# Kernel tuning notes

Measured on AMD Instinct MI355X. Metric: run time of the kernel, lower is better.

## Reference

```python
import jax, jax.numpy as jnp
import numpy as np

DIM = 768
HEADS = 12
E = 8
TOPK = 2
EPS = 1e-5


def layer_norm(x, g, b):
    m = jnp.mean(x, axis=-1, keepdims=True)
    v = jnp.mean((x - m) ** 2, axis=-1, keepdims=True)
    return (x - m) * jax.lax.rsqrt(v + EPS) * g + b


def setup_inputs() -> dict:
    key = jax.random.key(0)
    ks = jax.random.split(key, 12)
    B, N, C = 16, 1024, DIM
    s = 0.02
    return {
        "x": jax.random.normal(ks[0], (B, N, C), jnp.float32),
        "noise": jax.random.normal(ks[1], (B, N, E), jnp.float32),
        "ln1_g": jnp.ones((C,), jnp.float32),
        "ln1_b": jnp.zeros((C,), jnp.float32),
        "qkv_w": jax.random.normal(ks[2], (C, 3 * C), jnp.float32) * s,  # pre-transposed
        "proj_w": jax.random.normal(ks[3], (C, C), jnp.float32) * s,
        "proj_b": jnp.zeros((C,), jnp.float32),
        "ln2_g": jnp.ones((C,), jnp.float32),
        "ln2_b": jnp.zeros((C,), jnp.float32),
        "route_w": jax.random.normal(ks[4], (C, E), jnp.float32) * s,
        "route_b": jnp.zeros((E,), jnp.float32),
        "rln_g": jnp.ones((E,), jnp.float32),
        "rln_b": jnp.zeros((E,), jnp.float32),
        "expert_w": jax.random.normal(ks[5], (E, C, C), jnp.float32) * s,  # [E, in, out]
        "expert_b": jnp.zeros((E, C), jnp.float32),
    }


def reference(x, noise, ln1_g, ln1_b, qkv_w, proj_w, proj_b, ln2_g, ln2_b,
              route_w, route_b, rln_g, rln_b, expert_w, expert_b):
    B, N, C = x.shape
    H = HEADS
    Dh = C // H
    scale = Dh ** -0.5

    # --- Attention branch ---
    h = layer_norm(x, ln1_g, ln1_b)
    qkv = (h @ qkv_w).reshape(B, N, 3, H, Dh)
    q, k, v = qkv[:, :, 0], qkv[:, :, 1], qkv[:, :, 2]  # [B,N,H,Dh]
    attn = jnp.einsum('bnhd,bmhd->bhnm', q, k) * scale
    attn = jax.nn.softmax(attn, axis=-1)
    o = jnp.einsum('bhnm,bmhd->bnhd', attn, v).reshape(B, N, C)
    x = x + o @ proj_w + proj_b

    # --- MoE branch ---
    h = layer_norm(x, ln2_g, ln2_b)
    logits = layer_norm(h @ route_w + route_b, rln_g, rln_b)  # [B,N,E]
    rw = jax.nn.softmax(logits, axis=-1) + noise * (1.0 / E)
    topk_w, topk_idx = jax.lax.top_k(rw, TOPK)               # [B,N,K]
    topk_w = jax.nn.softmax(topk_w, axis=-1)

    # dense all-expert compute (faithful to source): [B,N,E,C]
    expert_out = jnp.einsum('bnc,ecd->bned', h, expert_w) + expert_b
    selected = jnp.take_along_axis(expert_out, topk_idx[..., None], axis=2)  # [B,N,K,C]
    moe = jnp.sum(selected * topk_w[..., None], axis=2)
    return x + moe
```

## Files before the change

### kernel.cpp

```cpp
#include <hip/hip_runtime.h>
#include <hip/hip_fp16.h>

typedef unsigned short u16;
typedef unsigned int u32;
typedef _Float16 f16;
typedef short bf16x8 __attribute__((ext_vector_type(8)));
typedef f16 f16x8 __attribute__((ext_vector_type(8)));
typedef float f32x4 __attribute__((ext_vector_type(4)));
typedef u32 u32x4 __attribute__((ext_vector_type(4)));

#define TOKENS 16384
#define CDIM 768
#define NEXP 8

__device__ __forceinline__ float b2f(u16 u) {
  return __uint_as_float(((u32)u) << 16);
}
__device__ __forceinline__ u16 f2b(float f) {
  u32 u = __float_as_uint(f);
  return (u16)((u + 0x7fffu + ((u >> 16) & 1u)) >> 16);
}
__device__ __forceinline__ f32x4 mfma_bf(bf16x8 a, bf16x8 b, f32x4 c) {
  return __builtin_amdgcn_mfma_f32_16x16x32_bf16(a, b, c, 0, 0, 0);
}
__device__ __forceinline__ f32x4 mfma_h(f16x8 a, f16x8 b, f32x4 c) {
  return __builtin_amdgcn_mfma_f32_16x16x32_f16(a, b, c, 0, 0, 0);
}
__device__ __forceinline__ void split8(const float* v, f16x8& h, f16x8& l) {
#pragma unroll
  for (int i = 0; i < 8; i++) {
    const f16 hh = (f16)v[i];
    h[i] = hh;
    l[i] = (f16)(v[i] - (float)hh);
  }
}

__global__ __launch_bounds__(256) void transpose_split_f16(
    const float* __restrict__ in, f16* __restrict__ oh, f16* __restrict__ ol,
    int K, int N) {
  __shared__ float tile[64][65];
  const int n0 = blockIdx.x * 64, k0 = blockIdx.y * 64;
#pragma unroll
  for (int i = 0; i < 16; i++) {
    const int s = threadIdx.x + i * 256;
    const int r = s >> 6, c = s & 63;
    tile[r][c] = in[(size_t)(k0 + r) * N + n0 + c];
  }
  __syncthreads();
#pragma unroll
  for (int i = 0; i < 16; i++) {
    const int s = threadIdx.x + i * 256;
    const int r = s >> 6, c = s & 63;
    const float v = tile[c][r];
    const f16 h = (f16)v;
    oh[(size_t)(n0 + r) * K + k0 + c] = h;
    ol[(size_t)(n0 + r) * K + k0 + c] = (f16)(v - (float)h);
  }
}

__global__ __launch_bounds__(256) void transpose_f32_bf16(
    const float* __restrict__ in, u16* __restrict__ out, int K, int N) {
  __shared__ u16 tile[64][65];
  const int z = blockIdx.z;
  in += (size_t)z * K * N;
  out += (size_t)z * K * N;
  const int n0 = blockIdx.x * 64, k0 = blockIdx.y * 64;
#pragma unroll
  for (int i = 0; i < 16; i++) {
    const int s = threadIdx.x + i * 256;
    const int r = s >> 6, c = s & 63;
    tile[r][c] = f2b(in[(size_t)(k0 + r) * N + n0 + c]);
  }
  __syncthreads();
#pragma unroll
  for (int i = 0; i < 16; i++) {
    const int s = threadIdx.x + i * 256;
    const int r = s >> 6, c = s & 63;
    out[(size_t)(n0 + r) * K + k0 + c] = tile[c][r];
  }
}

template <bool BF16OUT>
__global__ __launch_bounds__(256) void ln_rows(const float* __restrict__ in,
                                               const float* __restrict__ g,
                                               const float* __restrict__ bt,
                                               void* __restrict__ out) {
  const int row = blockIdx.x * 4 + (threadIdx.x >> 6);
  const int lane = threadIdx.x & 63;
  const size_t base = (size_t)row * CDIM;
  float v[12];
  float s = 0.f, ss = 0.f;
#pragma unroll
  for (int j = 0; j < 12; j++) {
    const int idx = lane + j * 64;
    v[j] = in[base + idx];
    s += v[j];
    ss += v[j] * v[j];
  }
#pragma unroll
  for (int m = 1; m < 64; m <<= 1) {
    s += __shfl_xor(s, m);
    ss += __shfl_xor(ss, m);
  }
  const float mean = s * (1.f / CDIM);
  const float var = ss * (1.f / CDIM) - mean * mean;
  const float rs = rsqrtf(var + 1e-5f);
#pragma unroll
  for (int j = 0; j < 12; j++) {
    const int idx = lane + j * 64;
    const float y = (v[j] - mean) * rs * g[idx] + bt[idx];
    if (BF16OUT)
      ((u16*)out)[base + idx] = f2b(y);
    else
      ((float*)out)[base + idx] = y;
  }
}

template <int EPI>
__global__ __launch_bounds__(256) void gemm_f16s(
    const float* __restrict__ A, const f16* __restrict__ Bth,
    const f16* __restrict__ Btl, float* __restrict__ C, int M, int N, int K,
    const float* __restrict__ bias, const float* __restrict__ xres) {
  __shared__ f16 Ah[128 * 64];
  __shared__ f16 Al[128 * 64];
  __shared__ f16 Bh[128 * 64];
  __shared__ f16 Bl[128 * 64];
  const int tid = threadIdx.x;
  const int lane = tid & 63, wv = tid >> 6;
  const int wr = wv >> 1, wc = wv & 1;
  const int lm = lane & 15, lq = lane >> 4;
  const int m0 = blockIdx.y * 128, n0 = blockIdx.x * 128;
  f32x4 acc[4][4];
  const f32x4 z4 = {0.f, 0.f, 0.f, 0.f};
#pragma unroll
  for (int i = 0; i < 4; i++)
#pragma unroll
    for (int j = 0; j < 4; j++) acc[i][j] = z4;

  for (int k0 = 0; k0 < K; k0 += 64) {
    __syncthreads();
#pragma unroll
    for (int i = 0; i < 4; i++) {
      const int s = tid + i * 256;
      const int r = s >> 3, g = s & 7;
      float av[8];
      *(float4*)&av[0] = *(const float4*)(A + (size_t)(m0 + r) * K + k0 + g * 8);
      *(float4*)&av[4] =
          *(const float4*)(A + (size_t)(m0 + r) * K + k0 + g * 8 + 4);
      f16x8 hh, ll;
      split8(av, hh, ll);
      const int sw = r * 64 + ((g ^ (r & 7)) << 3);
      *(f16x8*)(&Ah[sw]) = hh;
      *(f16x8*)(&Al[sw]) = ll;
      *(f16x8*)(&Bh[sw]) = *(const f16x8*)(Bth + (size_t)(n0 + r) * K + k0 + g * 8);
      *(f16x8*)(&Bl[sw]) = *(const f16x8*)(Btl + (size_t)(n0 + r) * K + k0 + g * 8);
    }
    __syncthreads();
#pragma unroll
    for (int kx = 0; kx < 8; kx += 4) {
      f16x8 afh[4], afl[4], bfh[4], bfl[4];
#pragma unroll
      for (int i = 0; i < 4; i++) {
        const int ra = wr * 64 + i * 16 + lm;
        const int aw = ra * 64 + (((ra & 7) ^ (kx + lq)) << 3);
        afh[i] = *(const f16x8*)(&Ah[aw]);
        afl[i] = *(const f16x8*)(&Al[aw]);
        const int rb = wc * 64 + i * 16 + lm;
        const int bw = rb * 64 + (((rb & 7) ^ (kx + lq)) << 3);
        bfh[i] = *(const f16x8*)(&Bh[bw]);
        bfl[i] = *(const f16x8*)(&Bl[bw]);
      }
#pragma unroll
      for (int i = 0; i < 4; i++)
#pragma unroll
        for (int j = 0; j < 4; j++) {
          acc[i][j] = mfma_h(afh[i], bfh[j], acc[i][j]);
          acc[i][j] = mfma_h(afh[i], bfl[j], acc[i][j]);
          acc[i][j] = mfma_h(afl[i], bfh[j], acc[i][j]);
        }
    }
  }
#pragma unroll
  for (int i = 0; i < 4; i++)
#pragma unroll
    for (int r = 0; r < 4; r++) {
      const size_t row = m0 + wr * 64 + i * 16 + lq * 4 + r;
#pragma unroll
      for (int j = 0; j < 4; j++) {
        const int col = n0 + wc * 64 + j * 16 + lm;
        float v = acc[i][j][r];
        if (EPI == 1) v += bias[col] + xres[row * N + col];
        C[row * N + col] = v;
      }
    }
}

__global__ __launch_bounds__(256) void attn_f16s(const float* __restrict__ qkvf,
                                                 float* __restrict__ o,
                                                 int qb) {
  __shared__ f16 Kh[64 * 64];
  __shared__ f16 Kl[64 * 64];
  __shared__ f16 Vh[64 * 64];
  __shared__ f16 Vl[64 * 64];
  __shared__ f16 Ph[4 * 16 * 64];
  __shared__ f16 Pl[4 * 16 * 64];
  const int bz = blockIdx.z, h = blockIdx.y, qt = blockIdx.x;
  const int tid = threadIdx.x, wv = tid >> 6, lane = tid & 63;
  const int lm = lane & 15, lq = lane >> 4;

  f16x8 qh[2], ql[2];
  {
    const size_t qbase =
        (size_t)(bz * 1024 + qt * 64 + wv * 16 + lm) * 2304 + h * 64;
#pragma unroll
    for (int f = 0; f < 2; f++) {
      float v[8];
      *(float4*)&v[0] = *(const float4*)(qkvf + qbase + f * 32 + lq * 8);
      *(float4*)&v[4] = *(const float4*)(qkvf + qbase + f * 32 + lq * 8 + 4);
      split8(v, qh[f], ql[f]);
    }
  }
  const f32x4 z4 = {0.f, 0.f, 0.f, 0.f};
  f32x4 oacc[4];
#pragma unroll
  for (int jb = 0; jb < 4; jb++) oacc[jb] = z4;
  float mrun[4], lrun[4];
#pragma unroll
  for (int r = 0; r < 4; r++) {
    mrun[r] = -1e30f;
    lrun[r] = 0.f;
  }
  const int vd = tid & 63;
  const int vkg = tid >> 6;
  f16* pwh = &Ph[wv * 16 * 64];
  f16* pwl = &Pl[wv * 16 * 64];

  for (int kt = 0; kt < 16; kt++) {
    __syncthreads();
#pragma unroll
    for (int i = 0; i < 2; i++) {
      const int s2 = tid + i * 256;
      const int r = s2 >> 3, g = s2 & 7;
      const size_t kb =
          (size_t)(bz * 1024 + kt * 64 + r) * 2304 + 768 + h * 64 + g * 8;
      float v[8];
      *(float4*)&v[0] = *(const float4*)(qkvf + kb);
      *(float4*)&v[4] = *(const float4*)(qkvf + kb + 4);
      f16x8 hh, ll;
      split8(v, hh, ll);
      const int sw = r * 64 + ((g ^ (r & 7)) << 3);
      *(f16x8*)(&Kh[sw]) = hh;
      *(f16x8*)(&Kl[sw]) = ll;
    }
#pragma unroll
    for (int sseg = 0; sseg < 2; sseg++) {
      const int k0v = vkg * 16 + sseg * 8;
      float v[8];
#pragma unroll
      for (int j = 0; j < 8; j++)
        v[j] = qkvf[(size_t)(bz * 1024 + kt * 64 + k0v + j) * 2304 + 1536 +
                    h * 64 + vd];
      f16x8 hh, ll;
      split8(v, hh, ll);
      const int g = k0v >> 3;
      const int sw = vd * 64 + ((g ^ (vd & 7)) << 3);
      *(f16x8*)(&Vh[sw]) = hh;
      *(f16x8*)(&Vl[sw]) = ll;
    }
    __syncthreads();

    f32x4 sa[4];
#pragma unroll
    for (int j = 0; j < 4; j++) sa[j] = z4;
#pragma unroll
    for (int kx = 0; kx < 8; kx += 4) {
      const f16x8 ah = qh[kx >> 2], al = ql[kx >> 2];
#pragma unroll
      for (int j = 0; j < 4; j++) {
        const int rb = j * 16 + lm;
        const int bw = rb * 64 + (((rb & 7) ^ (kx + lq)) << 3);
        const f16x8 bh = *(const f16x8*)(&Kh[bw]);
        const f16x8 bl = *(const f16x8*)(&Kl[bw]);
        sa[j] = mfma_h(ah, bh, sa[j]);
        sa[j] = mfma_h(ah, bl, sa[j]);
        sa[j] = mfma_h(al, bh, sa[j]);
      }
    }
#pragma unroll
    for (int j = 0; j < 4; j++)
#pragma unroll
      for (int r = 0; r < 4; r++) sa[j][r] *= 0.125f;

#pragma unroll
    for (int r = 0; r < 4; r++) {
      float mx = fmaxf(fmaxf(sa[0][r], sa[1][r]), fmaxf(sa[2][r], sa[3][r]));
      mx = fmaxf(mx, __shfl_xor(mx, 1));
      mx = fmaxf(mx, __shfl_xor(mx, 2));
      mx = fmaxf(mx, __shfl_xor(mx, 4));
      mx = fmaxf(mx, __shfl_xor(mx, 8));
      const float mnew = fmaxf(mrun[r], mx);
      const float alpha = expf(mrun[r] - mnew);
      float ps = 0.f;
#pragma unroll
      for (int j = 0; j < 4; j++) {
        const float p = expf(sa[j][r] - mnew);
        sa[j][r] = p;
        ps += p;
      }
      ps += __shfl_xor(ps, 1);
      ps += __shfl_xor(ps, 2);
      ps += __shfl_xor(ps, 4);
      ps += __shfl_xor(ps, 8);
      lrun[r] = lrun[r] * alpha + ps;
      mrun[r] = mnew;
#pragma unroll
      for (int jb = 0; jb < 4; jb++) oacc[jb][r] *= alpha;
    }

#pragma unroll
    for (int j = 0; j < 4; j++)
#pragma unroll
      for (int r = 0; r < 4; r++) {
        const int qr = lq * 4 + r;
        const int key = j * 16 + lm;
        const int ad = qr * 64 + (((qr & 7) ^ (key >> 3)) << 3) + (key & 7);
        const float p = sa[j][r];
        const f16 ph = (f16)p;
        pwh[ad] = ph;
        pwl[ad] = (f16)(p - (float)ph);
      }
#pragma unroll
    for (int kx2 = 0; kx2 < 8; kx2 += 4) {
      const int pw = lm * 64 + (((lm & 7) ^ (kx2 + lq)) << 3);
      const f16x8 pah = *(const f16x8*)(&pwh[pw]);
      const f16x8 pal = *(const f16x8*)(&pwl[pw]);
#pragma unroll
      for (int jb = 0; jb < 4; jb++) {
        const int rb = jb * 16 + lm;
        const int vw = rb * 64 + (((rb & 7) ^ (kx2 + lq)) << 3);
        const f16x8 vh = *(const f16x8*)(&Vh[vw]);
        const f16x8 vl = *(const f16x8*)(&Vl[vw]);
        oacc[jb] = mfma_h(pah, vh, oacc[jb]);
        oacc[jb] = mfma_h(pah, vl, oacc[jb]);
        oacc[jb] = mfma_h(pal, vh, oacc[jb]);
      }
    }
  }
  const int gtok = (qb * 4 + bz) * 1024 + qt * 64;
#pragma unroll
  for (int r = 0; r < 4; r++) {
    const float inv = 1.f / lrun[r];
    const size_t row = (size_t)gtok + wv * 16 + lq * 4 + r;
#pragma unroll
    for (int jb = 0; jb < 4; jb++) {
      const int col = h * 64 + jb * 16 + lm;
      o[row * CDIM + col] = oacc[jb][r] * inv;
    }
  }
}

__global__ __launch_bounds__(256) void gemm_expert(
    const u16* __restrict__ A, const u16* __restrict__ Bt,
    __half* __restrict__ Cp, int N, int K, const float* __restrict__ bias,
    const int* __restrict__ counts, const int* __restrict__ eBase,
    const int* __restrict__ tokList, const float* __restrict__ wgtList) {
  __shared__ u16 As[128 * 64];
  __shared__ u16 Bs[128 * 64];
  const int did = blockIdx.x;
  const int e = did & 7;
  const int s = did >> 3;
  const int bx = s % 6;
  const int by = s / 6;
  const int cnt = counts[e];
  const int m0 = by * 128, n0 = bx * 128;
  if (m0 >= cnt) return;
  const int tid = threadIdx.x;
  const int lane = tid & 63, wv = tid >> 6;
  const int wr = wv >> 1, wc = wv & 1;
  const int lm = lane & 15, lq = lane >> 4;
  const u16* Bte = Bt + (size_t)e * N * K;
  const int* tokl = tokList + e * TOKENS;
  const float* wl = wgtList + e * TOKENS;
  const float* biasE = bias + e * N;
  const int base0 = eBase[e];

  const int r0 = tid >> 3, g = tid & 7;
  const int swz = (g ^ (r0 & 7)) << 3;
  const u16* ap[4];
  const u16* bp[4];
#pragma unroll
  for (int i = 0; i < 4; i++) {
    const int row = m0 + r0 + i * 32;
    const int tok = (row < cnt) ? tokl[row] : 0;
    ap[i] = A + (size_t)tok * K + g * 8;
    bp[i] = Bte + (size_t)(n0 + r0 + i * 32) * K + g * 8;
  }

  f32x4 acc[4][4];
  const f32x4 z4 = {0.f, 0.f, 0.f, 0.f};
#pragma unroll
  for (int i = 0; i < 4; i++)
#pragma unroll
    for (int j = 0; j < 4; j++) acc[i][j] = z4;

  u32x4 pa[4], pb[4];
#pragma unroll
  for (int i = 0; i < 4; i++) {
    pa[i] = *(const u32x4*)(ap[i]);
    pb[i] = *(const u32x4*)(bp[i]);
  }
#pragma unroll
  for (int i = 0; i < 4; i++) {
    *(u32x4*)(&As[(r0 + i * 32) * 64 + swz]) = pa[i];
    *(u32x4*)(&Bs[(r0 + i * 32) * 64 + swz]) = pb[i];
  }

  for (int k0 = 0; k0 < K; k0 += 64) {
    __syncthreads();
    const bool more = (k0 + 64) < K;
    if (more) {
#pragma unroll
      for (int i = 0; i < 4; i++) {
        pa[i] = *(const u32x4*)(ap[i] + k0 + 64);
        pb[i] = *(const u32x4*)(bp[i] + k0 + 64);
      }
    }
#pragma unroll
    for (int kx = 0; kx < 8; kx += 4) {
      bf16x8 af[4], bfv[4];
#pragma unroll
      for (int i = 0; i < 4; i++) {
        const int ra = wr * 64 + i * 16 + lm;
        af[i] = *(const bf16x8*)(&As[ra * 64 + (((ra & 7) ^ (kx + lq)) << 3)]);
        const int rb = wc * 64 + i * 16 + lm;
        bfv[i] = *(const bf16x8*)(&Bs[rb * 64 + (((rb & 7) ^ (kx + lq)) << 3)]);
      }
#pragma unroll
      for (int i = 0; i < 4; i++)
#pragma unroll
        for (int j = 0; j < 4; j++)
          acc[i][j] = mfma_bf(af[i], bfv[j], acc[i][j]);
    }
    __syncthreads();
    if (more) {
#pragma unroll
      for (int i = 0; i < 4; i++) {
        *(u32x4*)(&As[(r0 + i * 32) * 64 + swz]) = pa[i];
        *(u32x4*)(&Bs[(r0 + i * 32) * 64 + swz]) = pb[i];
      }
    }
  }
#pragma unroll
  for (int i = 0; i < 4; i++)
#pragma unroll
    for (int r = 0; r < 4; r++) {
      const int rowi = m0 + wr * 64 + i * 16 + lq * 4 + r;
      const bool live = (rowi < cnt);
      const float w = live ? wl[rowi] : 0.f;
      const size_t prow = live ? (size_t)(base0 + rowi) * (size_t)N : 0;
#pragma unroll
      for (int j = 0; j < 4; j++) {
        const int col = n0 + wc * 64 + j * 16 + lm;
        const float v = (acc[i][j][r] + biasE[col]) * w;
        const float vn = __shfl_xor(v, 1);
        if (live && (lm & 1) == 0) {
          *(__half2*)(Cp + prow + col) =
              __halves2half2(__float2half(v), __float2half(vn));
        }
      }
    }
}

__global__ __launch_bounds__(256) void router_kernel(
    const float* __restrict__ x2, const float* __restrict__ g2,
    const float* __restrict__ b2, const float* __restrict__ rw,
    const float* __restrict__ rb, const float* __restrict__ rlng,
    const float* __restrict__ rlnb, const float* __restrict__ noise,
    int* __restrict__ eidx, float* __restrict__ ewgt) {
  const int token = blockIdx.x * 4 + (threadIdx.x >> 6);
  const int lane = threadIdx.x & 63;
  const size_t base = (size_t)token * CDIM;
  float v[12];
  float s = 0.f, ss = 0.f;
#pragma unroll
  for (int j = 0; j < 12; j++) {
    const int idx = lane + j * 64;
    v[j] = x2[base + idx];
    s += v[j];
    ss += v[j] * v[j];
  }
#pragma unroll
  for (int m = 1; m < 64; m <<= 1) {
    s += __shfl_xor(s, m);
    ss += __shfl_xor(ss, m);
  }
  const float mean = s * (1.f / CDIM);
  const float var = ss * (1.f / CDIM) - mean * mean;
  const float rs = rsqrtf(var + 1e-5f);

  float acc[8];
#pragma unroll
  for (int e = 0; e < 8; e++) acc[e] = 0.f;
#pragma unroll
  for (int j = 0; j < 12; j++) {
    const int d = lane + j * 64;
    const float hv = (v[j] - mean) * rs * g2[d] + b2[d];
    const f32x4 w0v = *(const f32x4*)(rw + (size_t)d * 8);
    const f32x4 w1v = *(const f32x4*)(rw + (size_t)d * 8 + 4);
#pragma unroll
    for (int e = 0; e < 4; e++) {
      acc[e] += hv * w0v[e];
      acc[e + 4] += hv * w1v[e];
    }
  }
#pragma unroll
  for (int m = 1; m < 64; m <<= 1)
#pragma unroll
    for (int e = 0; e < 8; e++) acc[e] += __shfl_xor(acc[e], m);

  float y[8];
  float emean = 0.f;
#pragma unroll
  for (int e = 0; e < 8; e++) {
    y[e] = acc[e] + rb[e];
    emean += y[e];
  }
  emean *= 0.125f;
  float evar = 0.f;
#pragma unroll
  for (int e = 0; e < 8; e++) {
    const float d = y[e] - emean;
    evar += d * d;
  }
  evar *= 0.125f;
  const float ers = rsqrtf(evar + 1e-5f);
  float lg[8];
  float mx = -1e30f;
#pragma unroll
  for (int e = 0; e < 8; e++) {
    lg[e] = (y[e] - emean) * ers * rlng[e] + rlnb[e];
    mx = fmaxf(mx, lg[e]);
  }
  float se = 0.f;
#pragma unroll
  for (int e = 0; e < 8; e++) {
    lg[e] = expf(lg[e] - mx);
    se += lg[e];
  }
  const float inv = 1.f / se;
  float r2[8];
#pragma unroll
  for (int e = 0; e < 8; e++)
    r2[e] = lg[e] * inv + noise[(size_t)token * 8 + e] * 0.125f;

  int e0 = 0;
  float v0 = r2[0];
#pragma unroll
  for (int e = 1; e < 8; e++)
    if (r2[e] > v0) {
      v0 = r2[e];
      e0 = e;
    }
  int e1 = -1;
  float v1 = -1e30f;
#pragma unroll
  for (int e = 0; e < 8; e++)
    if (e != e0 && r2[e] > v1) {
      v1 = r2[e];
      e1 = e;
    }
  const float w0 = 1.f / (1.f + expf(v1 - v0));
  if (lane == 0) {
    eidx[token * 2] = e0;
    eidx[token * 2 + 1] = e1;
    ewgt[token * 2] = w0;
    ewgt[token * 2 + 1] = 1.f - w0;
  }
}

__global__ __launch_bounds__(256) void build_lists(
    const int* __restrict__ eidx, const float* __restrict__ ewgt,
    int* __restrict__ counts, int* __restrict__ tokL, float* __restrict__ wgtL,
    int* __restrict__ posL) {
  const int e = blockIdx.x;
  __shared__ int cnt;
  if (threadIdx.x == 0) cnt = 0;
  __syncthreads();
  const int lane = threadIdx.x & 63;
  for (int t = threadIdx.x; t < TOKENS; t += 256) {
#pragma unroll
    for (int k = 0; k < 2; k++) {
      const bool match = (eidx[t * 2 + k] == e);
      const unsigned long long mb = __ballot(match);
      if (mb) {
        const int leader = __ffsll((unsigned long long)mb) - 1;
        int base = 0;
        if (lane == leader) base = atomicAdd(&cnt, __popcll(mb));
        base = __shfl(base, leader);
        if (match) {
          const int rank = __popcll(mb & ((1ull << lane) - 1ull));
          tokL[e * TOKENS + base + rank] = t;
          wgtL[e * TOKENS + base + rank] = ewgt[t * 2 + k];
          posL[t * 2 + k] = base + rank;
        }
      }
    }
  }
  __syncthreads();
  if (threadIdx.x == 0) counts[e] = cnt;
}

__global__ void prefix_counts(const int* __restrict__ counts,
                              int* __restrict__ eBase) {
  if (threadIdx.x == 0) {
    int s = 0;
#pragma unroll
    for (int e = 0; e < NEXP; e++) {
      eBase[e] = s;
      s += counts[e];
    }
    eBase[NEXP] = s;
  }
}

__global__ __launch_bounds__(256) void combine_moe(
    float* __restrict__ x2, const __half* __restrict__ Cp,
    const int* __restrict__ eidx, const int* __restrict__ posL,
    const int* __restrict__ eBase) {
  const int t = blockIdx.x * 4 + (threadIdx.x >> 6);
  const int lane = threadIdx.x & 63;
  const int e0 = eidx[t * 2], e1 = eidx[t * 2 + 1];
  const size_t q0 = (size_t)(eBase[e0] + posL[t * 2]) * CDIM;
  const size_t q1 = (size_t)(eBase[e1] + posL[t * 2 + 1]) * CDIM;
  const size_t base = (size_t)t * CDIM;
#pragma unroll
  for (int j = 0; j < 12; j++) {
    const int d = lane + j * 64;
    const float m =
        __half2float(Cp[q0 + d]) + __half2float(Cp[q1 + d]);
    x2[base + d] += m;
  }
}

__global__ __launch_bounds__(256) void copy_f32(const float* __restrict__ in,
                                                float* __restrict__ out) {
  const int i = (blockIdx.x * 256 + threadIdx.x) * 4;
  *(float4*)(out + i) = *(const float4*)(in + i);
}

extern "C" void kernel_launch(void* const* d_in, const int* in_sizes, int n_in,
                              void* d_out, int out_size, void* d_ws,
                              size_t ws_size, hipStream_t stream) {
  const float* x = (const float*)d_in[0];
  const float* noise = (const float*)d_in[1];
  const float* ln1_g = (const float*)d_in[2];
  const float* ln1_b = (const float*)d_in[3];
  const float* qkv_w = (const float*)d_in[4];
  const float* proj_w = (const float*)d_in[5];
  const float* proj_b = (const float*)d_in[6];
  const float* ln2_g = (const float*)d_in[7];
  const float* ln2_b = (const float*)d_in[8];
  const float* route_w = (const float*)d_in[9];
  const float* route_b = (const float*)d_in[10];
  const float* rln_g = (const float*)d_in[11];
  const float* rln_b = (const float*)d_in[12];
  const float* expert_w = (const float*)d_in[13];
  const float* expert_b = (const float*)d_in[14];

  char* ws = (char*)d_ws;
  float* x2f = (float*)(ws);
  float* qkvf = (float*)(ws + 50331648);
  u16* exp_wt = (u16*)(ws + 50331648);
  u16* h2 = (u16*)(ws + 59768832);
  int* counts = (int*)(ws + 84934656);
  int* eBase = (int*)(ws + 84934784);
  int* eidx = (int*)(ws + 84934912);
  float* ewgt = (float*)(ws + 85065984);
  int* tokL = (int*)(ws + 85197056);
  float* wgtL = (float*)(ws + 85721344);
  int* posL = (int*)(ws + 86245632);
  f16* qkvw_h = (f16*)(ws + 88080384);
  f16* qkvw_l = (f16*)(ws + 91619328);
  f16* projw_h = (f16*)(ws + 95158272);
  f16* projw_l = (f16*)(ws + 96337920);
  float* h1f = (float*)d_out;
  __half* cperm = (__half*)d_out;

  const dim3 blk(256);
  transpose_split_f16<<<dim3(36, 12), blk, 0, stream>>>(qkv_w, qkvw_h, qkvw_l,
                                                        768, 2304);
  transpose_split_f16<<<dim3(12, 12), blk, 0, stream>>>(proj_w, projw_h,
                                                        projw_l, 768, 768);
  ln_rows<false><<<dim3(4096), blk, 0, stream>>>(x, ln1_g, ln1_b, h1f);
  for (int q = 0; q < 4; q++) {
    gemm_f16s<0><<<dim3(18, 32), blk, 0, stream>>>(
        h1f + (size_t)q * 4096 * 768, qkvw_h, qkvw_l, qkvf, 4096, 2304, 768,
        nullptr, nullptr);
    attn_f16s<<<dim3(16, 12, 4), blk, 0, stream>>>(qkvf, h1f, q);
  }
  gemm_f16s<1><<<dim3(6, 128), blk, 0, stream>>>(h1f, projw_h, projw_l, x2f,
                                                 16384, 768, 768, proj_b, x);
  ln_rows<true><<<dim3(4096), blk, 0, stream>>>(x2f, ln2_g, ln2_b, h2);
  transpose_f32_bf16<<<dim3(12, 12, 8), blk, 0, stream>>>(expert_w, exp_wt,
                                                          768, 768);
  router_kernel<<<dim3(4096), blk, 0, stream>>>(x2f, ln2_g, ln2_b, route_w,
                                                route_b, rln_g, rln_b, noise,
                                                eidx, ewgt);
  build_lists<<<dim3(8), blk, 0, stream>>>(eidx, ewgt, counts, tokL, wgtL,
                                           posL);
  prefix_counts<<<dim3(1), dim3(64), 0, stream>>>(counts, eBase);
  gemm_expert<<<dim3(6144), blk, 0, stream>>>(h2, exp_wt, cperm, 768, 768,
                                              expert_b, counts, eBase, tokL,
                                              wgtL);
  combine_moe<<<dim3(4096), blk, 0, stream>>>(x2f, cperm, eidx, posL, eBase);
  copy_f32<<<dim3(12288), blk, 0, stream>>>(x2f, (float*)d_out);
}
```

Baseline: 1.140 ms.

## Fuse f16 hi/lo split and softmax scale into QKV GEMM epilogue

The QKV GEMM now writes Q and K directly as split f16 high/low halves, with Q pre-multiplied by scale*log2(e), and writes V as packed hi/lo u32 pairs. Previously it wrote fp32 that the attention kernel split on every tile load. The attention kernel loads the pre-split halves, drops its per-score scaling, and uses exp2f. This removes repeated conversion work and shrinks intermediate traffic, because each key/value tile is reloaded by many query blocks. The cost is scattered 2-byte stores in the GEMM epilogue and a slightly different rounding order, since Q is scaled before the split.

```diff
diff --git a/kernel.cpp b/kernel.cpp
--- a/kernel.cpp
+++ b/kernel.cpp
@@ -13,12 +13,16 @@
 #define CDIM 768
 #define NEXP 8
 
-__device__ __forceinline__ float b2f(u16 u) {
-  return __uint_as_float(((u32)u) << 16);
-}
+#define QSCALE 0.18033688011112043f
+
 __device__ __forceinline__ u16 f2b(float f) {
   u32 u = __float_as_uint(f);
   return (u16)((u + 0x7fffu + ((u >> 16) & 1u)) >> 16);
+}
+__device__ __forceinline__ u16 f16bits(f16 x) {
+  union { f16 f; u16 u; } c;
+  c.f = x;
+  return c.u;
 }
 __device__ __forceinline__ f32x4 mfma_bf(bf16x8 a, bf16x8 b, f32x4 c) {
   return __builtin_amdgcn_mfma_f32_16x16x32_bf16(a, b, c, 0, 0, 0);
@@ -120,7 +124,8 @@
 __global__ __launch_bounds__(256) void gemm_f16s(
     const float* __restrict__ A, const f16* __restrict__ Bth,
     const f16* __restrict__ Btl, float* __restrict__ C, int M, int N, int K,
-    const float* __restrict__ bias, const float* __restrict__ xres) {
+    const float* __restrict__ bias, const float* __restrict__ xres,
+    f16* __restrict__ Oh, f16* __restrict__ Ol, u32* __restrict__ Ov) {
   __shared__ f16 Ah[128 * 64];
   __shared__ f16 Al[128 * 64];
   __shared__ f16 Bh[128 * 64];
@@ -189,15 +194,30 @@
       for (int j = 0; j < 4; j++) {
         const int col = n0 + wc * 64 + j * 16 + lm;
         float v = acc[i][j][r];
-        if (EPI == 1) v += bias[col] + xres[row * N + col];
-        C[row * N + col] = v;
-      }
-    }
-}
-
-__global__ __launch_bounds__(256) void attn_f16s(const float* __restrict__ qkvf,
-                                                 float* __restrict__ o,
-                                                 int qb) {
+        if constexpr (EPI == 0) {
+          C[row * N + col] = v;
+        } else if constexpr (EPI == 1) {
+          v += bias[col] + xres[row * N + col];
+          C[row * N + col] = v;
+        } else {
+          if (n0 < 768) v *= QSCALE;
+          const f16 hh = (f16)v;
+          const f16 ll = (f16)(v - (float)hh);
+          if (n0 < 1536) {
+            Oh[row * 1536 + col] = hh;
+            Ol[row * 1536 + col] = ll;
+          } else {
+            Ov[row * 768 + (col - 1536)] =
+                (u32)f16bits(hh) | ((u32)f16bits(ll) << 16);
+          }
+        }
+      }
+    }
+}
+
+__global__ __launch_bounds__(256) void attn_f16s(
+    const f16* __restrict__ qkh, const f16* __restrict__ qkl,
+    const u32* __restrict__ vI, float* __restrict__ o, int qb) {
   __shared__ f16 Kh[64 * 64];
   __shared__ f16 Kl[64 * 64];
   __shared__ f16 Vh[64 * 64];
@@ -210,14 +230,12 @@
 
   f16x8 qh[2], ql[2];
   {
-    const size_t qbase =
-        (size_t)(bz * 1024 + qt * 64 + wv * 16 + lm) * 2304 + h * 64;
+    const size_t qrow =
+        (size_t)(bz * 1024 + qt * 64 + wv * 16 + lm) * 1536 + h * 64;
 #pragma unroll
     for (int f = 0; f < 2; f++) {
-      float v[8];
-      *(float4*)&v[0] = *(const float4*)(qkvf + qbase + f * 32 + lq * 8);
-      *(float4*)&v[4] = *(const float4*)(qkvf + qbase + f * 32 + lq * 8 + 4);
-      split8(v, qh[f], ql[f]);
+      qh[f] = *(const f16x8*)(qkh + qrow + f * 32 + lq * 8);
+      ql[f] = *(const f16x8*)(qkl + qrow + f * 32 + lq * 8);
     }
   }
   const f32x4 z4 = {0.f, 0.f, 0.f, 0.f};
@@ -242,26 +260,22 @@
       const int s2 = tid + i * 256;
       const int r = s2 >> 3, g = s2 & 7;
       const size_t kb =
-          (size_t)(bz * 1024 + kt * 64 + r) * 2304 + 768 + h * 64 + g * 8;
-      float v[8];
-      *(float4*)&v[0] = *(const float4*)(qkvf + kb);
-      *(float4*)&v[4] = *(const float4*)(qkvf + kb + 4);
-      f16x8 hh, ll;
-      split8(v, hh, ll);
+          (size_t)(bz * 1024 + kt * 64 + r) * 1536 + 768 + h * 64 + g * 8;
       const int sw = r * 64 + ((g ^ (r & 7)) << 3);
-      *(f16x8*)(&Kh[sw]) = hh;
-      *(f16x8*)(&Kl[sw]) = ll;
+      *(f16x8*)(&Kh[sw]) = *(const f16x8*)(qkh + kb);
+      *(f16x8*)(&Kl[sw]) = *(const f16x8*)(qkl + kb);
     }
 #pragma unroll
     for (int sseg = 0; sseg < 2; sseg++) {
       const int k0v = vkg * 16 + sseg * 8;
-      float v[8];
-#pragma unroll
-      for (int j = 0; j < 8; j++)
-        v[j] = qkvf[(size_t)(bz * 1024 + kt * 64 + k0v + j) * 2304 + 1536 +
-                    h * 64 + vd];
       f16x8 hh, ll;
-      split8(v, hh, ll);
+#pragma unroll
+      for (int j = 0; j < 8; j++) {
+        const u32 w = vI[(size_t)(bz * 1024 + kt * 64 + k0v + j) * 768 +
+                         h * 64 + vd];
+        ((u16*)&hh)[j] = (u16)(w & 0xffffu);
+        ((u16*)&ll)[j] = (u16)(w >> 16);
+      }
       const int g = k0v >> 3;
       const int sw = vd * 64 + ((g ^ (vd & 7)) << 3);
       *(f16x8*)(&Vh[sw]) = hh;
@@ -286,10 +300,6 @@
         sa[j] = mfma_h(al, bh, sa[j]);
       }
     }
-#pragma unroll
-    for (int j = 0; j < 4; j++)
-#pragma unroll
-      for (int r = 0; r < 4; r++) sa[j][r] *= 0.125f;
 
 #pragma unroll
     for (int r = 0; r < 4; r++) {
@@ -299,11 +309,11 @@
       mx = fmaxf(mx, __shfl_xor(mx, 4));
       mx = fmaxf(mx, __shfl_xor(mx, 8));
       const float mnew = fmaxf(mrun[r], mx);
-      const float alpha = expf(mrun[r] - mnew);
+      const float alpha = exp2f(mrun[r] - mnew);
       float ps = 0.f;
 #pragma unroll
       for (int j = 0; j < 4; j++) {
-        const float p = expf(sa[j][r] - mnew);
+        const float p = exp2f(sa[j][r] - mnew);
         sa[j][r] = p;
         ps += p;
       }
@@ -669,7 +679,9 @@
 
   char* ws = (char*)d_ws;
   float* x2f = (float*)(ws);
-  float* qkvf = (float*)(ws + 50331648);
+  f16* qkh = (f16*)(ws + 50331648);
+  f16* qkl = (f16*)(ws + 62914560);
+  u32* vIq = (u32*)(ws + 75497472);
   u16* exp_wt = (u16*)(ws + 50331648);
   u16* h2 = (u16*)(ws + 59768832);
   int* counts = (int*)(ws + 84934656);
@@ -693,13 +705,14 @@
                                                         projw_l, 768, 768);
   ln_rows<false><<<dim3(4096), blk, 0, stream>>>(x, ln1_g, ln1_b, h1f);
   for (int q = 0; q < 4; q++) {
-    gemm_f16s<0><<<dim3(18, 32), blk, 0, stream>>>(
-        h1f + (size_t)q * 4096 * 768, qkvw_h, qkvw_l, qkvf, 4096, 2304, 768,
-        nullptr, nullptr);
-    attn_f16s<<<dim3(16, 12, 4), blk, 0, stream>>>(qkvf, h1f, q);
+    gemm_f16s<2><<<dim3(18, 32), blk, 0, stream>>>(
+        h1f + (size_t)q * 4096 * 768, qkvw_h, qkvw_l, nullptr, 4096, 2304,
+        768, nullptr, nullptr, qkh, qkl, vIq);
+    attn_f16s<<<dim3(16, 12, 4), blk, 0, stream>>>(qkh, qkl, vIq, h1f, q);
   }
   gemm_f16s<1><<<dim3(6, 128), blk, 0, stream>>>(h1f, projw_h, projw_l, x2f,
-                                                 16384, 768, 768, proj_b, x);
+                                                 16384, 768, 768, proj_b, x,
+                                                 nullptr, nullptr, nullptr);
   ln_rows<true><<<dim3(4096), blk, 0, stream>>>(x2f, ln2_g, ln2_b, h2);
   transpose_f32_bf16<<<dim3(12, 12, 8), blk, 0, stream>>>(expert_w, exp_wt,
                                                           768, 768);
```

Result: faster. 1.088 ms, median of 2 (-4.5%).
